# Kernel optimization log

Measured on AMD Instinct MI355X. Metric: run time of the kernel, lower is better.

## Reference

```python
import jax, jax.numpy as jnp
import numpy as np
import math

B, Q, K = 8, 1024, 1024
EMBED, DOWN, H = 2048, 512, 16
DH_DOWN = DOWN // H   # 32
DH = EMBED // H       # 128


def setup_inputs() -> dict:
    key = jax.random.key(0)
    ks = jax.random.split(key, 10)
    s_down = 1.0 / math.sqrt(DOWN)
    s_embed = 1.0 / math.sqrt(EMBED)
    return {
        "query": jax.random.normal(ks[0], (B, Q, DOWN), jnp.float32),
        "key": jax.random.normal(ks[1], (B, K, DOWN), jnp.float32),
        "value": jax.random.normal(ks[2], (B, K, EMBED), jnp.float32),
        "attention_mask": jnp.ones((B, 1, Q, K), jnp.float32),
        "qW": jax.random.normal(ks[3], (DOWN, DOWN), jnp.float32) * s_down,
        "qb": jnp.zeros((DOWN,), jnp.float32),
        "kW": jax.random.normal(ks[4], (DOWN, DOWN), jnp.float32) * s_down,
        "kb": jnp.zeros((DOWN,), jnp.float32),
        "vW": jax.random.normal(ks[5], (EMBED, EMBED), jnp.float32) * s_embed,
        "vb": jnp.zeros((EMBED,), jnp.float32),
    }


def reference(query, key, value, attention_mask, qW, qb, kW, kb, vW, vb):
    bsz, q_len, _ = query.shape
    k_len = key.shape[1]
    # Linear projections (torch Linear: x @ W.T + b), split heads -> [B,H,L,dh]
    q = (query @ qW.T + qb).reshape(bsz, q_len, H, DH_DOWN).transpose(0, 2, 1, 3)
    k = (key @ kW.T + kb).reshape(bsz, k_len, H, DH_DOWN).transpose(0, 2, 1, 3)
    v = (value @ vW.T + vb).reshape(bsz, k_len, H, DH).transpose(0, 2, 1, 3)
    # fp32 logits, scaled by sqrt(down_head_dim)
    logits = jnp.einsum("bhqd,bhkd->bhqk", q.astype(jnp.float32), k.astype(jnp.float32)) / math.sqrt(DH_DOWN)
    # masked_fill(mask==0, -10000) then additive
    mask = jnp.where(attention_mask == 0, jnp.float32(-10000.0), attention_mask)
    logits = logits + mask
    attn_weights = jax.nn.softmax(logits, axis=-1).astype(v.dtype)
    attn_output = jnp.einsum("bhqk,bhkd->bhqd", attn_weights, v)
    attn_output = attn_output.transpose(0, 2, 1, 3).reshape(bsz, q_len, -1)
    return attn_output, attn_weights
```

## Files before the change

kernel.cpp:

```cpp
#include <hip/hip_runtime.h>


typedef _Float16 f16;
typedef _Float16 f16x8 __attribute__((ext_vector_type(8)));
typedef _Float16 f16x4 __attribute__((ext_vector_type(4)));
typedef float f32x4 __attribute__((ext_vector_type(4)));
typedef float f32x8 __attribute__((ext_vector_type(8)));

template <int MODE>
__global__ __launch_bounds__(256) void proj_gemm(
    const float* __restrict__ X, const float* __restrict__ W,
    const float* __restrict__ bias, f16* __restrict__ Y, int K, int N) {
  __shared__ f16 Asf[4096];
  __shared__ f16 Bsf[4096];
  const int t = threadIdx.x;
  const int lane = t & 63;
  const int w = t >> 6;
  const int wm = w >> 1, wn = w & 1;
  const int quad = lane >> 4, col = lane & 15;
  const long m0 = (long)blockIdx.x * 128;
  const int n0 = blockIdx.y * 128;

  f32x4 acc[4][4];
#pragma unroll
  for (int i = 0; i < 4; ++i)
#pragma unroll
    for (int j = 0; j < 4; ++j) acc[i][j] = (f32x4){0.f, 0.f, 0.f, 0.f};

  for (int k0 = 0; k0 < K; k0 += 32) {
    __syncthreads();
#pragma unroll
    for (int half = 0; half < 2; ++half) {
      const int s = t + half * 256;
      const int row = s >> 2;
      const int kq = s & 3;
      f32x8 xa = *(const f32x8*)(X + (m0 + row) * (long)K + k0 + kq * 8);
      f32x8 wa = *(const f32x8*)(W + ((long)n0 + row) * (long)K + k0 + kq * 8);
      const int off = (((row >> 4) * 64) + (row & 15) + (kq << 4)) * 8;
      *(f16x8*)&Asf[off] = __builtin_convertvector(xa, f16x8);
      *(f16x8*)&Bsf[off] = __builtin_convertvector(wa, f16x8);
    }
    __syncthreads();
    f16x8 a[4], b[4];
#pragma unroll
    for (int i = 0; i < 4; ++i)
      a[i] = *(const f16x8*)&Asf[((wm * 4 + i) * 64 + lane) * 8];
#pragma unroll
    for (int j = 0; j < 4; ++j)
      b[j] = *(const f16x8*)&Bsf[((wn * 4 + j) * 64 + lane) * 8];
#pragma unroll
    for (int i = 0; i < 4; ++i)
#pragma unroll
      for (int j = 0; j < 4; ++j)
        acc[i][j] = __builtin_amdgcn_mfma_f32_16x16x32_f16(a[i], b[j], acc[i][j], 0, 0, 0);
  }

#pragma unroll
  for (int j = 0; j < 4; ++j) {
    const int gn = n0 + (wn * 4 + j) * 16 + col;
    const float bv = bias[gn];
#pragma unroll
    for (int i = 0; i < 4; ++i) {
      const long gm0 = m0 + (wm * 4 + i) * 16 + quad * 4;
      if (MODE == 0) {
#pragma unroll
        for (int r = 0; r < 4; ++r)
          Y[(gm0 + r) * (long)N + gn] = (f16)(acc[i][j][r] + bv);
      } else {
        const long bb = gm0 >> 10;
        const int kpos = (int)(gm0 & 1023);
        f16x4 ov;
#pragma unroll
        for (int r = 0; r < 4; ++r) ov[r] = (f16)(acc[i][j][r] + bv);
        *(f16x4*)&Y[(bb * 2048 + gn) * 1024 + kpos] = ov;
      }
    }
  }
}

__global__ __launch_bounds__(256) void attn_fused(
    const f16* __restrict__ qhat, const f16* __restrict__ khat,
    const f16* __restrict__ vhatT, const float* __restrict__ mask,
    float* __restrict__ outO, float* __restrict__ outW) {
  __shared__ f16 P[16 * 1024];
  __shared__ float lpart[4][16];
  __shared__ float linv16[16];

  const int t = threadIdx.x;
  const int lane = t & 63;
  const int w = t >> 6;
  const int quad = lane >> 4, col = lane & 15;
  const int qt = blockIdx.x;
  const int bh = blockIdx.y;
  const int b = bh >> 4, h = bh & 15;
  const int q0 = qt * 16;

  const f16x8 afrag = *(const f16x8*)(qhat +
      ((long)(b * 1024 + q0 + col)) * 512 + h * 32 + quad * 8);

  const float sc = 0.17677669529663687f;
  const f32x4 zero = {0.f, 0.f, 0.f, 0.f};
  float lacc[4] = {0.f, 0.f, 0.f, 0.f};

  for (int nt = w; nt < 64; nt += 4) {
    const f16x8 bfrag = *(const f16x8*)(khat +
        ((long)(b * 1024 + nt * 16 + col)) * 512 + h * 32 + quad * 8);
    f32x4 c = __builtin_amdgcn_mfma_f32_16x16x32_f16(afrag, bfrag, zero, 0, 0, 0);
    const int kpos = nt * 16 + col;
    const int g = kpos >> 3;
    const long mrow0 = (long)b * 1024 + q0 + quad * 4;
#pragma unroll
    for (int r = 0; r < 4; ++r) {
      float mv = mask[(mrow0 + r) * 1024 + kpos];
      mv = (mv == 0.0f) ? -10000.0f : mv;
      const float e = __expf(c[r] * sc + mv);
      lacc[r] += e;
      const int qrow = quad * 4 + r;
      P[qrow * 1024 + ((g ^ (qrow & 7)) << 3) + (kpos & 7)] = (f16)e;
    }
  }

#pragma unroll
  for (int r = 0; r < 4; ++r) {
    float v = lacc[r];
#pragma unroll
    for (int d = 1; d < 16; d <<= 1) v += __shfl_xor(v, d, 64);
    lacc[r] = v;
  }
  if (col == 0) {
#pragma unroll
    for (int r = 0; r < 4; ++r) lpart[w][quad * 4 + r] = lacc[r];
  }
  __syncthreads();
  if (t < 16)
    linv16[t] = 1.0f / (lpart[0][t] + lpart[1][t] + lpart[2][t] + lpart[3][t]);
  __syncthreads();

  float* wbase = outW + ((long)bh * 1024 + q0) * 1024;
#pragma unroll
  for (int i = 0; i < 8; ++i) {
    const int idx = i * 2048 + t * 8;
    const int row = idx >> 10;
    const int c0 = idx & 1023;
    const float li = linv16[row];
    const int poff = row * 1024 + ((((c0 >> 3) ^ (row & 7)) << 3));
    f16x8 pv = *(const f16x8*)&P[poff];
    f32x4 o0, o1;
    f16x8 pn;
#pragma unroll
    for (int r = 0; r < 4; ++r) {
      const float w0 = (float)pv[r] * li;
      const float w1 = (float)pv[r + 4] * li;
      o0[r] = w0; o1[r] = w1;
      pn[r] = (f16)w0; pn[r + 4] = (f16)w1;
    }
    *(f16x8*)&P[poff] = pn;
    *(f32x4*)&wbase[(long)row * 1024 + c0] = o0;
    *(f32x4*)&wbase[(long)row * 1024 + c0 + 4] = o1;
  }
  __syncthreads();

  f32x4 oacc[2];
  oacc[0] = zero; oacc[1] = zero;
  const f16* vbase = vhatT + ((long)b * 2048 + h * 128 + w * 32) * 1024;
  for (int kc = 0; kc < 32; ++kc) {
    f16x8 bf[2], af;
#pragma unroll
    for (int n2 = 0; n2 < 2; ++n2)
      bf[n2] = *(const f16x8*)&vbase[(long)(n2 * 16 + col) * 1024 + kc * 32 + quad * 8];
    {
      const int row = col;
      const int g = kc * 4 + quad;
      af = *(const f16x8*)&P[row * 1024 + ((g ^ (row & 7)) << 3)];
    }
#pragma unroll
    for (int n2 = 0; n2 < 2; ++n2)
      oacc[n2] = __builtin_amdgcn_mfma_f32_16x16x32_f16(af, bf[n2], oacc[n2], 0, 0, 0);
  }
#pragma unroll
  for (int n2 = 0; n2 < 2; ++n2)
#pragma unroll
    for (int r = 0; r < 4; ++r) {
      const int qrow = quad * 4 + r;
      outO[((long)(b * 1024 + q0 + qrow)) * 2048 + h * 128 + w * 32 + n2 * 16 + col] =
          oacc[n2][r];
    }
}

extern "C" void kernel_launch(void* const* d_in, const int* in_sizes, int n_in,
                              void* d_out, int out_size, void* d_ws, size_t ws_size,
                              hipStream_t stream) {
  const float* query = (const float*)d_in[0];
  const float* key   = (const float*)d_in[1];
  const float* value = (const float*)d_in[2];
  const float* mask  = (const float*)d_in[3];
  const float* qW = (const float*)d_in[4];
  const float* qb = (const float*)d_in[5];
  const float* kW = (const float*)d_in[6];
  const float* kb = (const float*)d_in[7];
  const float* vW = (const float*)d_in[8];
  const float* vb = (const float*)d_in[9];

  float* outO = (float*)d_out;
  float* outW = outO + (size_t)8 * 1024 * 2048;

  char* ws = (char*)d_ws;
  f16* qhat  = (f16*)ws;
  f16* khat  = (f16*)(ws + ((size_t)8 << 20));
  f16* vhatT = (f16*)(ws + ((size_t)16 << 20));

  proj_gemm<0><<<dim3(64, 4), 256, 0, stream>>>(query, qW, qb, qhat, 512, 512);
  proj_gemm<0><<<dim3(64, 4), 256, 0, stream>>>(key, kW, kb, khat, 512, 512);
  proj_gemm<1><<<dim3(64, 16), 256, 0, stream>>>(value, vW, vb, vhatT, 2048, 2048);
  attn_fused<<<dim3(64, 128), 256, 0, stream>>>(qhat, khat, vhatT, mask, outO, outW);
}
```

Baseline: 1.186 ms.

## Prefetch GEMM tiles, merge Q/K projections, defer softmax normalization in attention

The projection GEMM now uses register prefetch of the next K slice, so global loads overlap the MFMA work. The Q and K projections are merged into one launch, and the logit scale is folded into the Q projection output. The attention kernel runs P·V on the unnormalized probabilities and applies 1/l to the output instead of rewriting P. It then writes the weights and output with nontemporal stores, adds an occupancy hint, and unrolls loops with mask loads issued earlier. Folding the scale into fp16 Q and using unnormalized fp16 P for P·V shift numerical rounding slightly.

```diff
diff --git a/kernel.cpp b/kernel.cpp
--- a/kernel.cpp
+++ b/kernel.cpp
@@ -8,11 +8,10 @@
 typedef float f32x8 __attribute__((ext_vector_type(8)));
 
 template <int MODE>
-__global__ __launch_bounds__(256) void proj_gemm(
+__device__ __forceinline__ void proj_body(
     const float* __restrict__ X, const float* __restrict__ W,
-    const float* __restrict__ bias, f16* __restrict__ Y, int K, int N) {
-  __shared__ f16 Asf[4096];
-  __shared__ f16 Bsf[4096];
+    const float* __restrict__ bias, f16* __restrict__ Y, int K, int N,
+    float oscale, f16* Asf, f16* Bsf) {
   const int t = threadIdx.x;
   const int lane = t & 63;
   const int w = t >> 6;
@@ -27,20 +26,33 @@
 #pragma unroll
     for (int j = 0; j < 4; ++j) acc[i][j] = (f32x4){0.f, 0.f, 0.f, 0.f};
 
+  const int kq = t & 3;
+  const int row0 = t >> 2;
+  const int row1 = row0 + 64;
+  const float* xp0 = X + (m0 + row0) * (long)K + kq * 8;
+  const float* xp1 = X + (m0 + row1) * (long)K + kq * 8;
+  const float* wp0 = W + ((long)n0 + row0) * (long)K + kq * 8;
+  const float* wp1 = W + ((long)n0 + row1) * (long)K + kq * 8;
+  const int l0 = (((row0 >> 4) * 64) + (row0 & 15) + (kq << 4)) * 8;
+  const int l1 = (((row1 >> 4) * 64) + (row1 & 15) + (kq << 4)) * 8;
+
+  f32x8 xa0 = *(const f32x8*)xp0;
+  f32x8 xa1 = *(const f32x8*)xp1;
+  f32x8 wa0 = *(const f32x8*)wp0;
+  f32x8 wa1 = *(const f32x8*)wp1;
+
   for (int k0 = 0; k0 < K; k0 += 32) {
+    *(f16x8*)&Asf[l0] = __builtin_convertvector(xa0, f16x8);
+    *(f16x8*)&Asf[l1] = __builtin_convertvector(xa1, f16x8);
+    *(f16x8*)&Bsf[l0] = __builtin_convertvector(wa0, f16x8);
+    *(f16x8*)&Bsf[l1] = __builtin_convertvector(wa1, f16x8);
     __syncthreads();
-#pragma unroll
-    for (int half = 0; half < 2; ++half) {
-      const int s = t + half * 256;
-      const int row = s >> 2;
-      const int kq = s & 3;
-      f32x8 xa = *(const f32x8*)(X + (m0 + row) * (long)K + k0 + kq * 8);
-      f32x8 wa = *(const f32x8*)(W + ((long)n0 + row) * (long)K + k0 + kq * 8);
-      const int off = (((row >> 4) * 64) + (row & 15) + (kq << 4)) * 8;
-      *(f16x8*)&Asf[off] = __builtin_convertvector(xa, f16x8);
-      *(f16x8*)&Bsf[off] = __builtin_convertvector(wa, f16x8);
-    }
-    __syncthreads();
+    if (k0 + 32 < K) {
+      xa0 = *(const f32x8*)(xp0 + k0 + 32);
+      xa1 = *(const f32x8*)(xp1 + k0 + 32);
+      wa0 = *(const f32x8*)(wp0 + k0 + 32);
+      wa1 = *(const f32x8*)(wp1 + k0 + 32);
+    }
     f16x8 a[4], b[4];
 #pragma unroll
     for (int i = 0; i < 4; ++i)
@@ -53,6 +65,7 @@
 #pragma unroll
       for (int j = 0; j < 4; ++j)
         acc[i][j] = __builtin_amdgcn_mfma_f32_16x16x32_f16(a[i], b[j], acc[i][j], 0, 0, 0);
+    __syncthreads();
   }
 
 #pragma unroll
@@ -65,20 +78,42 @@
       if (MODE == 0) {
 #pragma unroll
         for (int r = 0; r < 4; ++r)
-          Y[(gm0 + r) * (long)N + gn] = (f16)(acc[i][j][r] + bv);
+          Y[(gm0 + r) * (long)N + gn] = (f16)((acc[i][j][r] + bv) * oscale);
       } else {
         const long bb = gm0 >> 10;
         const int kpos = (int)(gm0 & 1023);
         f16x4 ov;
 #pragma unroll
-        for (int r = 0; r < 4; ++r) ov[r] = (f16)(acc[i][j][r] + bv);
+        for (int r = 0; r < 4; ++r) ov[r] = (f16)((acc[i][j][r] + bv) * oscale);
         *(f16x4*)&Y[(bb * 2048 + gn) * 1024 + kpos] = ov;
       }
     }
   }
 }
 
-__global__ __launch_bounds__(256) void attn_fused(
+template <int MODE>
+__global__ __launch_bounds__(256) void proj_gemm(
+    const float* __restrict__ X, const float* __restrict__ W,
+    const float* __restrict__ bias, f16* __restrict__ Y, int K, int N,
+    float oscale) {
+  __shared__ f16 Asf[4096];
+  __shared__ f16 Bsf[4096];
+  proj_body<MODE>(X, W, bias, Y, K, N, oscale, Asf, Bsf);
+}
+
+__global__ __launch_bounds__(256) void proj_qk(
+    const float* __restrict__ Xq, const float* __restrict__ Wq, const float* __restrict__ bq,
+    const float* __restrict__ Xk, const float* __restrict__ Wk, const float* __restrict__ bk,
+    f16* __restrict__ Yq, f16* __restrict__ Yk, float qscale) {
+  __shared__ f16 Asf[4096];
+  __shared__ f16 Bsf[4096];
+  if (blockIdx.z == 0)
+    proj_body<0>(Xq, Wq, bq, Yq, 512, 512, qscale, Asf, Bsf);
+  else
+    proj_body<0>(Xk, Wk, bk, Yk, 512, 512, 1.0f, Asf, Bsf);
+}
+
+__global__ __launch_bounds__(256, 4) void attn_fused(
     const f16* __restrict__ qhat, const f16* __restrict__ khat,
     const f16* __restrict__ vhatT, const float* __restrict__ mask,
     float* __restrict__ outO, float* __restrict__ outW) {
@@ -98,22 +133,25 @@
   const f16x8 afrag = *(const f16x8*)(qhat +
       ((long)(b * 1024 + q0 + col)) * 512 + h * 32 + quad * 8);
 
-  const float sc = 0.17677669529663687f;
   const f32x4 zero = {0.f, 0.f, 0.f, 0.f};
   float lacc[4] = {0.f, 0.f, 0.f, 0.f};
-
-  for (int nt = w; nt < 64; nt += 4) {
-    const f16x8 bfrag = *(const f16x8*)(khat +
-        ((long)(b * 1024 + nt * 16 + col)) * 512 + h * 32 + quad * 8);
+  const long mrow0 = (long)b * 1024 + q0 + quad * 4;
+  const f16* kbase = khat + ((long)b * 1024 + col) * 512 + h * 32 + quad * 8;
+
+#pragma unroll 4
+  for (int it = 0; it < 16; ++it) {
+    const int nt = w + it * 4;
+    const f16x8 bfrag = *(const f16x8*)(kbase + (long)nt * 16 * 512);
+    const int kpos = nt * 16 + col;
+    float mv[4];
+#pragma unroll
+    for (int r = 0; r < 4; ++r) mv[r] = mask[(mrow0 + r) * 1024 + kpos];
     f32x4 c = __builtin_amdgcn_mfma_f32_16x16x32_f16(afrag, bfrag, zero, 0, 0, 0);
-    const int kpos = nt * 16 + col;
     const int g = kpos >> 3;
-    const long mrow0 = (long)b * 1024 + q0 + quad * 4;
 #pragma unroll
     for (int r = 0; r < 4; ++r) {
-      float mv = mask[(mrow0 + r) * 1024 + kpos];
-      mv = (mv == 0.0f) ? -10000.0f : mv;
-      const float e = __expf(c[r] * sc + mv);
+      const float m = (mv[r] == 0.0f) ? -10000.0f : mv[r];
+      const float e = __expf(c[r] + m);
       lacc[r] += e;
       const int qrow = quad * 4 + r;
       P[qrow * 1024 + ((g ^ (qrow & 7)) << 3) + (kpos & 7)] = (f16)e;
@@ -134,7 +172,31 @@
   __syncthreads();
   if (t < 16)
     linv16[t] = 1.0f / (lpart[0][t] + lpart[1][t] + lpart[2][t] + lpart[3][t]);
+
+  f32x4 oacc0 = zero, oacc1 = zero;
+  const f16* vbase = vhatT + ((long)b * 2048 + h * 128 + w * 32) * 1024;
+  const f16* vb0 = vbase + (long)col * 1024 + quad * 8;
+  const f16* vb1 = vbase + (long)(16 + col) * 1024 + quad * 8;
+  const int prow = col * 1024;
+  const int pxor = col & 7;
+#pragma unroll 4
+  for (int kc = 0; kc < 32; ++kc) {
+    const f16x8 b0 = *(const f16x8*)(vb0 + kc * 32);
+    const f16x8 b1 = *(const f16x8*)(vb1 + kc * 32);
+    const f16x8 af = *(const f16x8*)&P[prow + (((kc * 4 + quad) ^ pxor) << 3)];
+    oacc0 = __builtin_amdgcn_mfma_f32_16x16x32_f16(af, b0, oacc0, 0, 0, 0);
+    oacc1 = __builtin_amdgcn_mfma_f32_16x16x32_f16(af, b1, oacc1, 0, 0, 0);
+  }
   __syncthreads();
+
+#pragma unroll
+  for (int r = 0; r < 4; ++r) {
+    const float li = linv16[quad * 4 + r];
+    const long orow =
+        ((long)(b * 1024 + q0 + quad * 4 + r)) * 2048 + h * 128 + w * 32 + col;
+    __builtin_nontemporal_store(oacc0[r] * li, &outO[orow]);
+    __builtin_nontemporal_store(oacc1[r] * li, &outO[orow + 16]);
+  }
 
   float* wbase = outW + ((long)bh * 1024 + q0) * 1024;
 #pragma unroll
@@ -144,47 +206,16 @@
     const int c0 = idx & 1023;
     const float li = linv16[row];
     const int poff = row * 1024 + ((((c0 >> 3) ^ (row & 7)) << 3));
-    f16x8 pv = *(const f16x8*)&P[poff];
+    const f16x8 pv = *(const f16x8*)&P[poff];
     f32x4 o0, o1;
-    f16x8 pn;
 #pragma unroll
     for (int r = 0; r < 4; ++r) {
-      const float w0 = (float)pv[r] * li;
-      const float w1 = (float)pv[r + 4] * li;
-      o0[r] = w0; o1[r] = w1;
-      pn[r] = (f16)w0; pn[r + 4] = (f16)w1;
-    }
-    *(f16x8*)&P[poff] = pn;
-    *(f32x4*)&wbase[(long)row * 1024 + c0] = o0;
-    *(f32x4*)&wbase[(long)row * 1024 + c0 + 4] = o1;
-  }
-  __syncthreads();
-
-  f32x4 oacc[2];
-  oacc[0] = zero; oacc[1] = zero;
-  const f16* vbase = vhatT + ((long)b * 2048 + h * 128 + w * 32) * 1024;
-  for (int kc = 0; kc < 32; ++kc) {
-    f16x8 bf[2], af;
-#pragma unroll
-    for (int n2 = 0; n2 < 2; ++n2)
-      bf[n2] = *(const f16x8*)&vbase[(long)(n2 * 16 + col) * 1024 + kc * 32 + quad * 8];
-    {
-      const int row = col;
-      const int g = kc * 4 + quad;
-      af = *(const f16x8*)&P[row * 1024 + ((g ^ (row & 7)) << 3)];
-    }
-#pragma unroll
-    for (int n2 = 0; n2 < 2; ++n2)
-      oacc[n2] = __builtin_amdgcn_mfma_f32_16x16x32_f16(af, bf[n2], oacc[n2], 0, 0, 0);
-  }
-#pragma unroll
-  for (int n2 = 0; n2 < 2; ++n2)
-#pragma unroll
-    for (int r = 0; r < 4; ++r) {
-      const int qrow = quad * 4 + r;
-      outO[((long)(b * 1024 + q0 + qrow)) * 2048 + h * 128 + w * 32 + n2 * 16 + col] =
-          oacc[n2][r];
-    }
+      o0[r] = (float)pv[r] * li;
+      o1[r] = (float)pv[r + 4] * li;
+    }
+    __builtin_nontemporal_store(o0, (f32x4*)&wbase[(long)row * 1024 + c0]);
+    __builtin_nontemporal_store(o1, (f32x4*)&wbase[(long)row * 1024 + c0 + 4]);
+  }
 }
 
 extern "C" void kernel_launch(void* const* d_in, const int* in_sizes, int n_in,
@@ -209,8 +240,9 @@
   f16* khat  = (f16*)(ws + ((size_t)8 << 20));
   f16* vhatT = (f16*)(ws + ((size_t)16 << 20));
 
-  proj_gemm<0><<<dim3(64, 4), 256, 0, stream>>>(query, qW, qb, qhat, 512, 512);
-  proj_gemm<0><<<dim3(64, 4), 256, 0, stream>>>(key, kW, kb, khat, 512, 512);
-  proj_gemm<1><<<dim3(64, 16), 256, 0, stream>>>(value, vW, vb, vhatT, 2048, 2048);
+  const float sc = 0.17677669529663687f;
+  proj_qk<<<dim3(64, 4, 2), 256, 0, stream>>>(query, qW, qb, key, kW, kb,
+                                              qhat, khat, sc);
+  proj_gemm<1><<<dim3(64, 16), 256, 0, stream>>>(value, vW, vb, vhatT, 2048, 2048, 1.0f);
   attn_fused<<<dim3(64, 128), 256, 0, stream>>>(qhat, khat, vhatT, mask, outO, outW);
 }
```

After: 1.086 ms. 1.09x faster.
